# Kernel tuning notes

Hardware: AMD Instinct MI355X
Metric: run time of the kernel (lower is better)

## Reference

```python
import jax, jax.numpy as jnp
import numpy as np

D = 2048
NH = 16
DH = D // NH            # 128
DHR = DH // 2           # 64
DC = D // 2             # 1024
DCQ = D // 2            # 1024
B, L = 4, 2048
ROPE_BASE = 10000.0


def setup_inputs() -> dict:
    key = jax.random.key(0)
    ks = jax.random.split(key, 10)
    s = 0.02
    inp = {
        "x": jax.random.normal(ks[0], (B, L, D), dtype=jnp.float32),
        "W_DKV": jax.random.normal(ks[1], (D, DC), dtype=jnp.float32) * s,
        "W_UK": jax.random.normal(ks[2], (DC, NH * DH), dtype=jnp.float32) * s,
        "W_UV": jax.random.normal(ks[3], (DC, NH * DH), dtype=jnp.float32) * s,
        "W_DQ": jax.random.normal(ks[4], (D, DCQ), dtype=jnp.float32) * s,
        "W_UQ": jax.random.normal(ks[5], (DCQ, NH * DH), dtype=jnp.float32) * s,
        "W_QR": jax.random.normal(ks[6], (DCQ, NH * DHR), dtype=jnp.float32) * s,
        "W_KR": jax.random.normal(ks[7], (D, DHR), dtype=jnp.float32) * s,
        "W_O": jax.random.normal(ks[8], (D, D), dtype=jnp.float32) * s,
        "s_qk": jnp.asarray(np.sqrt(DH + DHR), dtype=jnp.float32),
    }
    return inp


def _rope_tables(seq_len, dim, dtype):
    # Standard rotate-half RoPE tables: cos/sin of shape (seq_len, dim)
    inv_freq = 1.0 / (ROPE_BASE ** (jnp.arange(0, dim, 2, dtype=jnp.float32) / dim))
    t = jnp.arange(seq_len, dtype=jnp.float32)
    freqs = jnp.outer(t, inv_freq)            # (L, dim/2)
    emb = jnp.concatenate([freqs, freqs], axis=-1)  # (L, dim)
    return jnp.cos(emb).astype(dtype), jnp.sin(emb).astype(dtype)


def _apply_rope(x, cos, sin):
    # x: (B, H, L, dim); cos/sin: (L, dim)
    half = x.shape[-1] // 2
    rot = jnp.concatenate([-x[..., half:], x[..., :half]], axis=-1)
    return x * cos[None, None] + rot * sin[None, None]


def reference(x, W_DKV, W_UK, W_UV, W_DQ, W_UQ, W_QR, W_KR, W_O, s_qk):
    Bb, Ll, Dd = x.shape
    cos, sin = _rope_tables(Ll, DHR, x.dtype)

    c_kv = x @ W_DKV                                            # (B,L,DC)
    k_c = (c_kv @ W_UK).reshape(Bb, Ll, NH, DH).transpose(0, 2, 1, 3)
    v = (c_kv @ W_UV).reshape(Bb, Ll, NH, DH).transpose(0, 2, 1, 3)

    c_q = x @ W_DQ                                              # (B,L,DCQ)
    q_c = (c_q @ W_UQ).reshape(Bb, Ll, NH, DH).transpose(0, 2, 1, 3)
    q_rope = _apply_rope((c_q @ W_QR).reshape(Bb, Ll, NH, DHR).transpose(0, 2, 1, 3), cos, sin)
    k_rope = _apply_rope((x @ W_KR).reshape(Bb, Ll, 1, DHR).transpose(0, 2, 1, 3), cos, sin)
    k_rope = jnp.broadcast_to(k_rope, (Bb, NH, Ll, DHR))

    q = jnp.concatenate([q_c, q_rope], axis=-1)                 # (B,H,L,DH+DHR)
    k = jnp.concatenate([k_c, k_rope], axis=-1)

    eps = 1e-12
    q = q / jnp.maximum(jnp.linalg.norm(q, axis=-1, keepdims=True), eps)
    k = k / jnp.maximum(jnp.linalg.norm(k, axis=-1, keepdims=True), eps)

    # SDPA with scale=1.0, causal mask, q pre-scaled by s_qk
    scores = jnp.einsum("bhqd,bhkd->bhqk", q * s_qk, k)         # (B,H,L,L)
    causal = jnp.tril(jnp.ones((Ll, Ll), dtype=bool))
    scores = jnp.where(causal[None, None], scores, jnp.finfo(scores.dtype).min)
    attn = jax.nn.softmax(scores, axis=-1)
    out = jnp.einsum("bhqk,bhkd->bhqd", attn, v)                # (B,H,L,DH)
    out = out.transpose(0, 2, 1, 3).reshape(Bb, Ll, Dd)
    return out @ W_O
```

## Files before the change

### kernel.cpp

```cpp
#include <hip/hip_runtime.h>
#include <stdint.h>

typedef unsigned short u16;
typedef unsigned int u32;
typedef short bf16x8 __attribute__((ext_vector_type(8)));
typedef float f32x4 __attribute__((ext_vector_type(4)));
typedef u16 u16x4 __attribute__((ext_vector_type(4)));

#define DEV __device__ __forceinline__

DEV float bf2f(u16 u) { union { float f; u32 i; } x; x.i = ((u32)u) << 16; return x.f; }
DEV u16 f2bf(float f) {
  union { float f; u32 i; } x; x.f = f;
  u32 i = x.i;
  u32 r = (i + 0x7fffu + ((i >> 16) & 1u)) >> 16;
  return (u16)r;
}

DEV void gl_lds16(const u16* g, u16* l) {
  __builtin_amdgcn_global_load_lds((const __attribute__((address_space(1))) u32*)g,
                                   (__attribute__((address_space(3))) u32*)l, 16, 0, 0);
}

__global__ __launch_bounds__(256) void cast_f32_bf16(const float* __restrict__ in,
                                                     u16* __restrict__ out, int n4) {
  int i = blockIdx.x * 256 + threadIdx.x;
  if (i >= n4) return;
  float4 v = ((const float4*)in)[i];
  u16x4 o;
  o.x = f2bf(v.x); o.y = f2bf(v.y); o.z = f2bf(v.z); o.w = f2bf(v.w);
  ((u16x4*)out)[i] = o;
}

__global__ __launch_bounds__(256) void transpose_cast(const float* __restrict__ W,
                                                      u16* __restrict__ Wt, int K, int N) {
  __shared__ float tile[64][65];
  int n0 = blockIdx.x * 64;
  int k0 = blockIdx.y * 64;
#pragma unroll
  for (int i = 0; i < 16; ++i) {
    int idx = threadIdx.x + i * 256;
    int r = idx >> 6, c = idx & 63;
    tile[r][c] = W[(size_t)(k0 + r) * N + n0 + c];
  }
  __syncthreads();
#pragma unroll
  for (int i = 0; i < 16; ++i) {
    int idx = threadIdx.x + i * 256;
    int r = idx >> 6, c = idx & 63;
    Wt[(size_t)(n0 + r) * K + k0 + c] = f2bf(tile[c][r]);
  }
}

__global__ __launch_bounds__(256) void transpose_v(const u16* __restrict__ KCV,
                                                   u16* __restrict__ Vt) {
  __shared__ float tile[64][65];
  int l0 = blockIdx.x * 64;
  int d0 = blockIdx.y * 64;
  int bh = blockIdx.z;
  int b = bh >> 4, h = bh & 15;
#pragma unroll
  for (int i = 0; i < 16; ++i) {
    int idx = threadIdx.x + i * 256;
    int r = idx >> 6, c = idx & 63;
    tile[r][c] = bf2f(KCV[(size_t)(b * 2048 + l0 + r) * 4096 + 2048 + h * 128 + d0 + c]);
  }
  __syncthreads();
#pragma unroll
  for (int i = 0; i < 16; ++i) {
    int idx = threadIdx.x + i * 256;
    int rr = idx >> 6, cc = idx & 63;
    Vt[((size_t)bh * 128 + d0 + rr) * 2048 + l0 + cc] = f2bf(tile[cc][rr]);
  }
}

DEV void ep_set(u16* E, int i, float v) { E[i] = f2bf(v); }
DEV void ep_set(float* E, int i, float v) { E[i] = v; }

template <typename OT>
__global__ __launch_bounds__(512, 2) void gemm256(const u16* __restrict__ A, int lda,
                                                  const u16* __restrict__ Bt,
                                                  OT* __restrict__ C, int ldc, int K) {
  __shared__ u16 smem[65536];
  const int tid = threadIdx.x;
  const int lane = tid & 63;
  const int w = tid >> 6;
  const int wm = w >> 2;
  const int wn = w & 3;
  const int quad = lane >> 4;
  const int l15 = lane & 15;
  const int cs = quad ^ ((l15 >> 1) & 3);
  const int nwg = gridDim.x * gridDim.y;
  const int lin = blockIdx.y * gridDim.x + blockIdx.x;
  const int swz = (lin & 7) * (nwg >> 3) + (lin >> 3);
  const int m0 = (swz / gridDim.x) * 256;
  const int n0 = (swz % gridDim.x) * 256;

  const int rloc = tid >> 2;
  const int clog = (tid & 3) ^ ((tid >> 3) & 3);
  const size_t aoff0 = (size_t)rloc * lda + clog * 8;
  const size_t boff0 = (size_t)rloc * (size_t)K + clog * 8;
  const u16* Ag = A + (size_t)m0 * lda;
  const u16* Bg = Bt + (size_t)n0 * K;

  auto stageA = [&](int u, int ks2) {
    u16* dst = smem + (u & 1) * 32768 + ks2 * 8192 + w * 512;
    const u16* s0 = Ag + aoff0 + u * 64 + ks2 * 32;
    gl_lds16(s0, dst);
    gl_lds16(s0 + (size_t)128 * lda, dst + 4096);
  };
  auto stageB = [&](int u, int ks2) {
    u16* dst = smem + (u & 1) * 32768 + 16384 + ks2 * 8192 + w * 512;
    const u16* s0 = Bg + boff0 + u * 64 + ks2 * 32;
    gl_lds16(s0, dst);
    gl_lds16(s0 + (size_t)128 * (size_t)K, dst + 4096);
  };

  f32x4 acc[2][4][4] = {};
  const int nt = K >> 6;

  stageA(0, 0); stageB(0, 0); stageA(0, 1); stageB(0, 1);
  stageA(1, 0); stageB(1, 0);
  asm volatile("s_waitcnt vmcnt(4)" ::: "memory");
  __builtin_amdgcn_s_barrier();

  for (int t = 0; t < nt; ++t) {
    const u16* As_ = smem + (t & 1) * 32768;
    const u16* Bs_ = As_ + 16384;
#pragma unroll
    for (int p = 0; p < 4; ++p) {
      const int ks = p >> 1;
      const int mq = p & 1;
      const u16* Ab = As_ + ks * 8192;
      const u16* Bb = Bs_ + ks * 8192;
      bf16x8 af[4], bf[4];
#pragma unroll
      for (int mt = 0; mt < 4; ++mt)
        af[mt] = *(const bf16x8*)&Ab[(wm * 128 + mq * 64 + mt * 16 + l15) * 32 + cs * 8];
#pragma unroll
      for (int n = 0; n < 4; ++n)
        bf[n] = *(const bf16x8*)&Bb[(wn * 64 + n * 16 + l15) * 32 + cs * 8];
      if (p == 0)      { if (t + 1 < nt) stageA(t + 1, 1); }
      else if (p == 1) { if (t + 1 < nt) stageB(t + 1, 1); }
      else if (p == 2) { if (t + 2 < nt) stageA(t + 2, 0); }
      else             { if (t + 2 < nt) stageB(t + 2, 0); }
      __builtin_amdgcn_s_barrier();
      __builtin_amdgcn_s_setprio(1);
#pragma unroll
      for (int mt = 0; mt < 4; ++mt)
#pragma unroll
        for (int n = 0; n < 4; ++n)
          acc[mq][mt][n] = __builtin_amdgcn_mfma_f32_16x16x32_bf16(af[mt], bf[n], acc[mq][mt][n], 0, 0, 0);
      __builtin_amdgcn_s_setprio(0);
      if (p == 3) asm volatile("s_waitcnt vmcnt(4)" ::: "memory");
      __builtin_amdgcn_s_barrier();
    }
  }
  asm volatile("s_waitcnt vmcnt(0)" ::: "memory");
  __builtin_amdgcn_s_barrier();

  OT* Ew = ((OT*)smem) + w * 1024;
#pragma unroll
  for (int mq = 0; mq < 2; ++mq) {
#pragma unroll
    for (int mt = 0; mt < 4; ++mt) {
#pragma unroll
      for (int n = 0; n < 4; ++n)
#pragma unroll
        for (int r = 0; r < 4; ++r)
          ep_set(Ew, (quad * 4 + r) * 64 + n * 16 + l15, acc[mq][mt][n][r]);
      asm volatile("s_waitcnt lgkmcnt(0)" ::: "memory");
#pragma unroll
      for (int it2 = 0; it2 < 4; ++it2) {
        int row_i = it2 * 4 + quad;
        size_t off = (size_t)(m0 + wm * 128 + mq * 64 + mt * 16 + row_i) * ldc + n0 + wn * 64 + l15 * 4;
        if constexpr (sizeof(OT) == 2) {
          *(u16x4*)&C[off] = *(const u16x4*)&Ew[row_i * 64 + l15 * 4];
        } else {
          *(float4*)&C[off] = *(const float4*)&Ew[row_i * 64 + l15 * 4];
        }
      }
      asm volatile("s_waitcnt lgkmcnt(0)" ::: "memory");
    }
  }
}

template <typename OT>
__global__ __launch_bounds__(256) void gemm_bt(const u16* __restrict__ A, int lda,
                                               const u16* __restrict__ Bt,
                                               OT* __restrict__ C, int ldc,
                                               int M, int N, int K) {
  __shared__ u16 smem_ab[2 * 128 * 32];
  u16* As = smem_ab;
  u16* Bs = smem_ab + 128 * 32;
  const int tid = threadIdx.x;
  const int lane = tid & 63;
  const int w = tid >> 6;
  const int quad = lane >> 4;
  const int l15 = lane & 15;
  const int nwg = gridDim.x * gridDim.y;
  const int lin = blockIdx.y * gridDim.x + blockIdx.x;
  const int swz = (lin & 7) * (nwg >> 3) + (lin >> 3);
  const int m0 = (swz / gridDim.x) * 128;
  const int n0 = (swz % gridDim.x) * 128;
  const int wm = (w & 1) * 64;
  const int wn = (w >> 1) * 64;

  f32x4 acc[4][4] = {};

  for (int k0 = 0; k0 < K; k0 += 32) {
#pragma unroll
    for (int it = 0; it < 2; ++it) {
      int ca = w * 128 + it * 64;
      int c = ca + lane;
      int row = c >> 2, kc = (c & 3) * 8;
      gl_lds16(A + (size_t)(m0 + row) * lda + k0 + kc, &As[ca * 8]);
      gl_lds16(Bt + (size_t)(n0 + row) * K + k0 + kc, &Bs[ca * 8]);
    }
    __syncthreads();
    bf16x8 af[4], bf[4];
#pragma unroll
    for (int mt = 0; mt < 4; ++mt) af[mt] = *(const bf16x8*)&As[(wm + mt * 16 + l15) * 32 + quad * 8];
#pragma unroll
    for (int nt = 0; nt < 4; ++nt) bf[nt] = *(const bf16x8*)&Bs[(wn + nt * 16 + l15) * 32 + quad * 8];
#pragma unroll
    for (int mt = 0; mt < 4; ++mt)
#pragma unroll
      for (int nt = 0; nt < 4; ++nt)
        acc[mt][nt] = __builtin_amdgcn_mfma_f32_16x16x32_bf16(af[mt], bf[nt], acc[mt][nt], 0, 0, 0);
    __syncthreads();
  }

  OT* Ew = ((OT*)smem_ab) + w * 1024;
#pragma unroll
  for (int mt = 0; mt < 4; ++mt) {
#pragma unroll
    for (int nt = 0; nt < 4; ++nt)
#pragma unroll
      for (int r = 0; r < 4; ++r)
        ep_set(Ew, (quad * 4 + r) * 64 + nt * 16 + l15, acc[mt][nt][r]);
    asm volatile("s_waitcnt lgkmcnt(0)" ::: "memory");
#pragma unroll
    for (int it2 = 0; it2 < 4; ++it2) {
      int row_i = it2 * 4 + quad;
      int colg = n0 + wn + l15 * 4;
      if (colg < N) {
        size_t off = (size_t)(m0 + wm + mt * 16 + row_i) * ldc + colg;
        if constexpr (sizeof(OT) == 2) {
          *(u16x4*)&C[off] = *(const u16x4*)&Ew[row_i * 64 + l15 * 4];
        } else {
          *(float4*)&C[off] = *(const float4*)&Ew[row_i * 64 + l15 * 4];
        }
      }
    }
    asm volatile("s_waitcnt lgkmcnt(0)" ::: "memory");
  }
}

__global__ __launch_bounds__(256) void build_q(const u16* __restrict__ qcr,
                                               const float* __restrict__ s_qk,
                                               u16* __restrict__ qn) {
  const int wid = blockIdx.x * 4 + (threadIdx.x >> 6);
  const int lane = threadIdx.x & 63;
  const int token = wid >> 4;
  const int h = wid & 15;
  const int b = token >> 11;
  const int l = token & 2047;
  float v0 = bf2f(qcr[(size_t)token * 3072 + h * 128 + lane]);
  float v1 = bf2f(qcr[(size_t)token * 3072 + h * 128 + 64 + lane]);
  int j = lane & 31;
  float freq = __expf((float)j * -0.28782313662425574f);
  float ang = (float)l * freq;
  float cs = __cosf(ang), sn = __sinf(ang);
  float xr = bf2f(qcr[(size_t)token * 3072 + 2048 + h * 64 + lane]);
  float xo = bf2f(qcr[(size_t)token * 3072 + 2048 + h * 64 + (lane ^ 32)]);
  float v2 = (lane < 32) ? (xr * cs - xo * sn) : (xr * cs + xo * sn);
  float ss = v0 * v0 + v1 * v1 + v2 * v2;
#pragma unroll
  for (int off = 1; off < 64; off <<= 1) ss += __shfl_xor(ss, off, 64);
  float scale = s_qk[0] / fmaxf(sqrtf(ss), 1e-12f);
  u16* out = qn + (((size_t)(b * 16 + h) * 2048) + l) * 192;
  out[lane] = f2bf(v0 * scale);
  out[64 + lane] = f2bf(v1 * scale);
  out[128 + lane] = f2bf(v2 * scale);
}

__global__ __launch_bounds__(256) void build_k(const u16* __restrict__ kcv,
                                               const u16* __restrict__ krr,
                                               u16* __restrict__ kn) {
  const int wid = blockIdx.x * 4 + (threadIdx.x >> 6);
  const int lane = threadIdx.x & 63;
  const int token = wid >> 4;
  const int h = wid & 15;
  const int b = token >> 11;
  const int l = token & 2047;
  float v0 = bf2f(kcv[(size_t)token * 4096 + h * 128 + lane]);
  float v1 = bf2f(kcv[(size_t)token * 4096 + h * 128 + 64 + lane]);
  int j = lane & 31;
  float freq = __expf((float)j * -0.28782313662425574f);
  float ang = (float)l * freq;
  float cs = __cosf(ang), sn = __sinf(ang);
  float xr = bf2f(krr[(size_t)token * 64 + lane]);
  float xo = bf2f(krr[(size_t)token * 64 + (lane ^ 32)]);
  float v2 = (lane < 32) ? (xr * cs - xo * sn) : (xr * cs + xo * sn);
  float ss = v0 * v0 + v1 * v1 + v2 * v2;
#pragma unroll
  for (int off = 1; off < 64; off <<= 1) ss += __shfl_xor(ss, off, 64);
  float scale = 1.0f / fmaxf(sqrtf(ss), 1e-12f);
  u16* out = kn + (((size_t)(b * 16 + h) * 2048) + l) * 192;
  out[lane] = f2bf(v0 * scale);
  out[64 + lane] = f2bf(v1 * scale);
  out[128 + lane] = f2bf(v2 * scale);
}

__global__ __launch_bounds__(512, 2) void flash_attn(const u16* __restrict__ Q,
                                                     const u16* __restrict__ Kn,
                                                     const u16* __restrict__ Vt,
                                                     const float* __restrict__ s_qk,
                                                     u16* __restrict__ O) {
  constexpr int L = 2048, DQK = 192, DV = 128, KVB = 64;
  constexpr int PSTR = 72;
  __shared__ u16 smem[59392];
  u16* KsBuf = smem;
  u16* VsBuf = smem + 24576;
  u16* Ps    = smem + 40960;
  const int tid = threadIdx.x;
  const int lane = tid & 63;
  const int w = tid >> 6;
  const int quad = lane >> 4;
  const int l15 = lane & 15;
  const int lin = blockIdx.x;
  const int xcd = lin & 7;
  const int g = lin >> 3;
  const int bh = ((g >> 2) << 3) | xcd;
  const int pairIdx = g & 3;
  const int b = bh >> 4, h = bh & 15;
  const float SMAX = s_qk[0];

  const u16* Kg = Kn + (size_t)bh * L * DQK;
  const u16* Vg = Vt + (size_t)bh * DV * L;

  auto stage = [&](int kt2, int bufi) {
    u16* KsB = KsBuf + bufi * 12288;
    u16* VsB = VsBuf + bufi * 8192;
#pragma unroll
    for (int it = 0; it < 5; ++it) {
      int B0 = it * 512 + w * 64;
      if (B0 < 1536) {
        int p = B0 + lane;
        int r = p / 24, cp = p % 24;
        int c = cp ^ (r & 7);
        gl_lds16(Kg + (size_t)(kt2 * KVB + r) * DQK + c * 8, &KsB[B0 * 8]);
      } else {
        int p = B0 - 1536 + lane;
        int dv = p >> 3, cp = p & 7;
        int c = cp ^ (dv & 7);
        gl_lds16(Vg + (size_t)dv * L + kt2 * KVB + c * 8, &VsB[(B0 - 1536) * 8]);
      }
    }
  };

  bf16x8 ones;
#pragma unroll
  for (int j = 0; j < 8; ++j) ones[j] = (short)0x3F80;

  for (int qp = 0; qp < 2; ++qp) {
    const int qt = (qp == 0) ? (7 - pairIdx) : pairIdx;
    const u16* Qg = Q + ((size_t)bh * L + qt * 256) * DQK;

    bf16x8 qf[2][6];
#pragma unroll
    for (int mt = 0; mt < 2; ++mt)
#pragma unroll
      for (int kd = 0; kd < 6; ++kd)
        qf[mt][kd] = *(const bf16x8*)&Qg[(w * 32 + mt * 16 + l15) * DQK + kd * 32 + quad * 8];

    f32x4 oacc[2][8] = {};
    f32x4 accL[2] = {};

    const int nkv = 4 * (qt + 1);
    stage(0, 0);
    __syncthreads();

    for (int kt = 0; kt < nkv; ++kt) {
      const int cur = kt & 1;
      if (kt + 1 < nkv) stage(kt + 1, cur ^ 1);
      const u16* KsC = KsBuf + cur * 12288;
      const u16* VsC = VsBuf + cur * 8192;

      f32x4 s[2][4] = {};
      __builtin_amdgcn_s_setprio(1);
#pragma unroll
      for (int kd = 0; kd < 6; ++kd) {
#pragma unroll
        for (int nt = 0; nt < 4; ++nt) {
          int row = nt * 16 + l15;
          int cp = (kd * 4 + quad) ^ (l15 & 7);
          bf16x8 bb = *(const bf16x8*)&KsC[row * DQK + cp * 8];
#pragma unroll
          for (int mt = 0; mt < 2; ++mt)
            s[mt][nt] = __builtin_amdgcn_mfma_f32_16x16x32_bf16(qf[mt][kd], bb, s[mt][nt], 0, 0, 0);
        }
      }
      __builtin_amdgcn_s_setprio(0);

      const int kcol0 = kt * KVB + l15;
      u16* Pw = &Ps[w * 32 * PSTR];
#pragma unroll
      for (int mt = 0; mt < 2; ++mt) {
        const int qrow_base = qt * 256 + w * 32 + mt * 16 + quad * 4;
#pragma unroll
        for (int r = 0; r < 4; ++r)
#pragma unroll
          for (int nt = 0; nt < 4; ++nt) {
            float p = (kcol0 + nt * 16 > qrow_base + r) ? 0.f : __expf(s[mt][nt][r] - SMAX);
            Pw[(mt * 16 + quad * 4 + r) * PSTR + nt * 16 + l15] = f2bf(p);
          }
      }
      asm volatile("s_waitcnt lgkmcnt(0)" ::: "memory");

      __builtin_amdgcn_s_setprio(1);
      bf16x8 pf[2][2];
#pragma unroll
      for (int mt = 0; mt < 2; ++mt)
#pragma unroll
        for (int kc = 0; kc < 2; ++kc) {
          pf[mt][kc] = *(const bf16x8*)&Pw[(mt * 16 + l15) * PSTR + kc * 32 + quad * 8];
          accL[mt] = __builtin_amdgcn_mfma_f32_16x16x32_bf16(pf[mt][kc], ones, accL[mt], 0, 0, 0);
        }
#pragma unroll
      for (int nt2 = 0; nt2 < 8; ++nt2) {
        const int dv = nt2 * 16 + l15;
#pragma unroll
        for (int kc = 0; kc < 2; ++kc) {
          int lc = (kc * 4 + quad) ^ (l15 & 7);
          bf16x8 vv = *(const bf16x8*)&VsC[dv * KVB + lc * 8];
#pragma unroll
          for (int mt = 0; mt < 2; ++mt)
            oacc[mt][nt2] = __builtin_amdgcn_mfma_f32_16x16x32_bf16(pf[mt][kc], vv, oacc[mt][nt2], 0, 0, 0);
        }
      }
      __builtin_amdgcn_s_setprio(0);
      __syncthreads();
    }

    float rinv[2][4];
#pragma unroll
    for (int mt = 0; mt < 2; ++mt)
#pragma unroll
      for (int r = 0; r < 4; ++r) rinv[mt][r] = 1.0f / accL[mt][r];
    u16* Ew = smem + w * 2048;
#pragma unroll
    for (int mt = 0; mt < 2; ++mt) {
#pragma unroll
      for (int nt2 = 0; nt2 < 8; ++nt2)
#pragma unroll
        for (int r = 0; r < 4; ++r)
          Ew[(quad * 4 + r) * 128 + nt2 * 16 + l15] = f2bf(oacc[mt][nt2][r] * rinv[mt][r]);
      asm volatile("s_waitcnt lgkmcnt(0)" ::: "memory");
#pragma unroll
      for (int it2 = 0; it2 < 4; ++it2) {
        int row_i = it2 * 4 + quad;
        int lg = qt * 256 + w * 32 + mt * 16 + row_i;
        uint4 v = *(const uint4*)&Ew[row_i * 128 + l15 * 8];
        *(uint4*)&O[((size_t)b * L + lg) * 2048 + h * 128 + l15 * 8] = v;
      }
      asm volatile("s_waitcnt lgkmcnt(0)" ::: "memory");
    }
    __syncthreads();
  }
}

extern "C" void kernel_launch(void* const* d_in, const int* in_sizes, int n_in,
                              void* d_out, int out_size, void* d_ws, size_t ws_size,
                              hipStream_t stream) {
  const float* x     = (const float*)d_in[0];
  const float* W_DKV = (const float*)d_in[1];
  const float* W_UK  = (const float*)d_in[2];
  const float* W_UV  = (const float*)d_in[3];
  const float* W_DQ  = (const float*)d_in[4];
  const float* W_UQ  = (const float*)d_in[5];
  const float* W_QR  = (const float*)d_in[6];
  const float* W_KR  = (const float*)d_in[7];
  const float* W_O   = (const float*)d_in[8];
  const float* s_qk  = (const float*)d_in[9];

  char* base = (char*)d_ws;
  u16* xb     = (u16*)(base);
  u16* WtDKVQ = (u16*)(base + (size_t)33554432);
  u16* WtUKV  = (u16*)(base + (size_t)41943040);
  u16* WtUQR  = (u16*)(base + (size_t)58720256);
  u16* WtKR   = (u16*)(base + (size_t)71303168);
  u16* WtO    = (u16*)(base + (size_t)71827456);
  u16* ckvq   = (u16*)(base + (size_t)80216064);
  u16* kcv    = (u16*)(base + (size_t)113770496);
  u16* qcr    = (u16*)(base + (size_t)180879360);
  u16* kr     = (u16*)(base + (size_t)231211008);
  u16* qn = (u16*)(base);
  u16* kn = qcr;
  u16* Vt = ckvq;
  u16* O  = kcv;

  cast_f32_bf16<<<16384, 256, 0, stream>>>(x, xb, 8192 * 2048 / 4);
  transpose_cast<<<dim3(16, 32), 256, 0, stream>>>(W_DKV, WtDKVQ,                  2048, 1024);
  transpose_cast<<<dim3(16, 32), 256, 0, stream>>>(W_DQ,  WtDKVQ + 1024 * 2048,    2048, 1024);
  transpose_cast<<<dim3(32, 16), 256, 0, stream>>>(W_UK,  WtUKV,                   1024, 2048);
  transpose_cast<<<dim3(32, 16), 256, 0, stream>>>(W_UV,  WtUKV + 2048 * 1024,     1024, 2048);
  transpose_cast<<<dim3(32, 16), 256, 0, stream>>>(W_UQ,  WtUQR,                   1024, 2048);
  transpose_cast<<<dim3(16, 16), 256, 0, stream>>>(W_QR,  WtUQR + 2048 * 1024,     1024, 1024);
  transpose_cast<<<dim3(1, 32),  256, 0, stream>>>(W_KR,  WtKR,                    2048, 64);
  transpose_cast<<<dim3(32, 32), 256, 0, stream>>>(W_O,   WtO,                     2048, 2048);

  gemm256<u16><<<dim3(8, 32),  512, 0, stream>>>(xb, 2048, WtDKVQ, ckvq, 2048, 2048);
  gemm_bt<u16><<<dim3(1, 64),  256, 0, stream>>>(xb, 2048, WtKR, kr, 64, 8192, 64, 2048);
  gemm256<u16><<<dim3(16, 32), 512, 0, stream>>>(ckvq, 2048, WtUKV, kcv, 4096, 1024);
  gemm256<u16><<<dim3(12, 32), 512, 0, stream>>>(ckvq + 1024, 2048, WtUQR, qcr, 3072, 1024);

  build_q<<<32768, 256, 0, stream>>>(qcr, s_qk, qn);
  build_k<<<32768, 256, 0, stream>>>(kcv, kr, kn);

  transpose_v<<<dim3(32, 2, 64), 256, 0, stream>>>(kcv, Vt);

  flash_attn<<<dim3(256), 512, 0, stream>>>(qn, kn, Vt, s_qk, O);

  gemm256<float><<<dim3(8, 32), 512, 0, stream>>>(O, 2048, WtO, (float*)d_out, 2048, 2048);
}
```

Baseline: 678.2 us.

## Fuse prep casts, merge projection GEMMs, and fold V transpose and Q norm

All input casts and weight transposes now run in a single prep kernel. The small W_KR projection is folded into the first GEMM as an extra zero-padded N tile, and the K/V/Q up-projections are merged into one GEMM launch. That GEMM writes V directly in transposed layout from its epilogue, so the separate transpose_v kernel goes away. The Q RoPE and normalization move into flash_attn's Q load, removing build_q and its intermediate buffer. The aim is fewer launches and less intermediate memory traffic, at the cost of extra per-tile Q work inside attention and more complex epilogues.

```diff
diff --git a/kernel.cpp b/kernel.cpp
--- a/kernel.cpp
+++ b/kernel.cpp
@@ -22,65 +22,77 @@
                                    (__attribute__((address_space(3))) u32*)l, 16, 0, 0);
 }
 
-__global__ __launch_bounds__(256) void cast_f32_bf16(const float* __restrict__ in,
-                                                     u16* __restrict__ out, int n4) {
-  int i = blockIdx.x * 256 + threadIdx.x;
-  if (i >= n4) return;
-  float4 v = ((const float4*)in)[i];
-  u16x4 o;
-  o.x = f2bf(v.x); o.y = f2bf(v.y); o.z = f2bf(v.z); o.w = f2bf(v.w);
-  ((u16x4*)out)[i] = o;
-}
-
-__global__ __launch_bounds__(256) void transpose_cast(const float* __restrict__ W,
-                                                      u16* __restrict__ Wt, int K, int N) {
+__global__ __launch_bounds__(256) void prep(const float* __restrict__ x,
+                                            const float* __restrict__ W_DKV,
+                                            const float* __restrict__ W_UK,
+                                            const float* __restrict__ W_UV,
+                                            const float* __restrict__ W_DQ,
+                                            const float* __restrict__ W_UQ,
+                                            const float* __restrict__ W_QR,
+                                            const float* __restrict__ W_KR,
+                                            const float* __restrict__ W_O,
+                                            u16* __restrict__ xb,
+                                            u16* __restrict__ WtDKVQ,
+                                            u16* __restrict__ WtUKV,
+                                            u16* __restrict__ WtO) {
   __shared__ float tile[64][65];
-  int n0 = blockIdx.x * 64;
-  int k0 = blockIdx.y * 64;
+  const int tid = threadIdx.x;
+  int bid = blockIdx.x;
+
+  if (bid < 4096) {
+#pragma unroll
+    for (int it = 0; it < 4; ++it) {
+      int i = bid * 1024 + it * 256 + tid;
+      float4 v = ((const float4*)x)[i];
+      u16x4 o;
+      o.x = f2bf(v.x); o.y = f2bf(v.y); o.z = f2bf(v.z); o.w = f2bf(v.w);
+      ((u16x4*)xb)[i] = o;
+    }
+    return;
+  }
+  bid -= 4096;
+
+  const float* W; u16* Wt; int K, N;
+  if (bid < 512)        { W = W_DKV; Wt = WtDKVQ;                K = 2048; N = 1024; }
+  else if (bid < 1024)  { W = W_DQ;  Wt = WtDKVQ + 1024 * 2048;  K = 2048; N = 1024; bid -= 512; }
+  else if (bid < 1536)  { W = W_UK;  Wt = WtUKV;                 K = 1024; N = 2048; bid -= 1024; }
+  else if (bid < 2048)  { W = W_UV;  Wt = WtUKV + 2048 * 1024;   K = 1024; N = 2048; bid -= 1536; }
+  else if (bid < 2560)  { W = W_UQ;  Wt = WtUKV + 4096 * 1024;   K = 1024; N = 2048; bid -= 2048; }
+  else if (bid < 2816)  { W = W_QR;  Wt = WtUKV + 6144 * 1024;   K = 1024; N = 1024; bid -= 2560; }
+  else if (bid < 2848)  { W = W_KR;  Wt = WtDKVQ + 2048 * 2048;  K = 2048; N = 64;   bid -= 2816; }
+  else if (bid < 3040) {
+    int i = (bid - 2848) * 256 + tid;
+    *(uint4*)&WtDKVQ[2112 * 2048 + i * 8] = uint4{0, 0, 0, 0};
+    return;
+  }
+  else                  { W = W_O;   Wt = WtO;                   K = 2048; N = 2048; bid -= 3040; }
+
+  const int gx = N >> 6;
+  const int n0 = (bid % gx) * 64;
+  const int k0 = (bid / gx) * 64;
 #pragma unroll
   for (int i = 0; i < 16; ++i) {
-    int idx = threadIdx.x + i * 256;
+    int idx = tid + i * 256;
     int r = idx >> 6, c = idx & 63;
     tile[r][c] = W[(size_t)(k0 + r) * N + n0 + c];
   }
   __syncthreads();
 #pragma unroll
   for (int i = 0; i < 16; ++i) {
-    int idx = threadIdx.x + i * 256;
+    int idx = tid + i * 256;
     int r = idx >> 6, c = idx & 63;
     Wt[(size_t)(n0 + r) * K + k0 + c] = f2bf(tile[c][r]);
   }
 }
 
-__global__ __launch_bounds__(256) void transpose_v(const u16* __restrict__ KCV,
-                                                   u16* __restrict__ Vt) {
-  __shared__ float tile[64][65];
-  int l0 = blockIdx.x * 64;
-  int d0 = blockIdx.y * 64;
-  int bh = blockIdx.z;
-  int b = bh >> 4, h = bh & 15;
-#pragma unroll
-  for (int i = 0; i < 16; ++i) {
-    int idx = threadIdx.x + i * 256;
-    int r = idx >> 6, c = idx & 63;
-    tile[r][c] = bf2f(KCV[(size_t)(b * 2048 + l0 + r) * 4096 + 2048 + h * 128 + d0 + c]);
-  }
-  __syncthreads();
-#pragma unroll
-  for (int i = 0; i < 16; ++i) {
-    int idx = threadIdx.x + i * 256;
-    int rr = idx >> 6, cc = idx & 63;
-    Vt[((size_t)bh * 128 + d0 + rr) * 2048 + l0 + cc] = f2bf(tile[cc][rr]);
-  }
-}
-
 DEV void ep_set(u16* E, int i, float v) { E[i] = f2bf(v); }
 DEV void ep_set(float* E, int i, float v) { E[i] = v; }
 
-template <typename OT>
+template <typename OT, int KIND>
 __global__ __launch_bounds__(512, 2) void gemm256(const u16* __restrict__ A, int lda,
                                                   const u16* __restrict__ Bt,
-                                                  OT* __restrict__ C, int ldc, int K) {
+                                                  OT* __restrict__ C, int ldc, int K,
+                                                  u16* __restrict__ X1, u16* __restrict__ X2) {
   __shared__ u16 smem[65536];
   const int tid = threadIdx.x;
   const int lane = tid & 63;
@@ -98,9 +110,10 @@
 
   const int rloc = tid >> 2;
   const int clog = (tid & 3) ^ ((tid >> 3) & 3);
+  const u16* Abase = A + ((KIND == 2 && n0 >= 4096) ? 1024 : 0);
   const size_t aoff0 = (size_t)rloc * lda + clog * 8;
   const size_t boff0 = (size_t)rloc * (size_t)K + clog * 8;
-  const u16* Ag = A + (size_t)m0 * lda;
+  const u16* Ag = Abase + (size_t)m0 * lda;
   const u16* Bg = Bt + (size_t)n0 * K;
 
   auto stageA = [&](int u, int ks2) {
@@ -159,6 +172,44 @@
   asm volatile("s_waitcnt vmcnt(0)" ::: "memory");
   __builtin_amdgcn_s_barrier();
 
+  if constexpr (KIND == 2) {
+    if (n0 >= 2048 && n0 < 4096) {
+      u16* Ewt = smem + w * 2560;
+      const int dvb = (n0 - 2048) + wn * 64;
+      const int hh = dvb >> 7;
+      const int dv0 = dvb & 127;
+#pragma unroll
+      for (int mq = 0; mq < 2; ++mq)
+#pragma unroll
+        for (int mh = 0; mh < 2; ++mh) {
+#pragma unroll
+          for (int mi = 0; mi < 2; ++mi)
+#pragma unroll
+            for (int n = 0; n < 4; ++n)
+#pragma unroll
+              for (int r = 0; r < 4; ++r)
+                Ewt[(n * 16 + l15) * 40 + mi * 16 + quad * 4 + r] = f2bf(acc[mq][mh * 2 + mi][n][r]);
+          asm volatile("s_waitcnt lgkmcnt(0)" ::: "memory");
+          const int mbase = m0 + wm * 128 + mq * 64 + mh * 32;
+          const int b_ = mbase >> 11, l_ = mbase & 2047;
+          u16* dstp = X1 + ((size_t)((b_ * 16 + hh) * 128 + dv0 + lane)) * 2048 + l_;
+          const u16* srcp = &Ewt[lane * 40];
+#pragma unroll
+          for (int k2 = 0; k2 < 4; ++k2)
+            *(uint4*)&dstp[k2 * 8] = *(const uint4*)&srcp[k2 * 8];
+          asm volatile("s_waitcnt lgkmcnt(0)" ::: "memory");
+        }
+      return;
+    }
+  }
+
+  OT* Cc = C; int ldcc = ldc, col0 = n0, Nlim = 1 << 30;
+  if constexpr (KIND == 1) {
+    if (n0 == 2048) { Cc = (OT*)X1; ldcc = 64; col0 = 0; Nlim = 64; }
+  }
+  if constexpr (KIND == 2) {
+    if (n0 >= 4096) { Cc = (OT*)X2; ldcc = 3072; col0 = n0 - 4096; }
+  }
   OT* Ew = ((OT*)smem) + w * 1024;
 #pragma unroll
   for (int mq = 0; mq < 2; ++mq) {
@@ -173,11 +224,14 @@
 #pragma unroll
       for (int it2 = 0; it2 < 4; ++it2) {
         int row_i = it2 * 4 + quad;
-        size_t off = (size_t)(m0 + wm * 128 + mq * 64 + mt * 16 + row_i) * ldc + n0 + wn * 64 + l15 * 4;
-        if constexpr (sizeof(OT) == 2) {
-          *(u16x4*)&C[off] = *(const u16x4*)&Ew[row_i * 64 + l15 * 4];
-        } else {
-          *(float4*)&C[off] = *(const float4*)&Ew[row_i * 64 + l15 * 4];
+        int colg = wn * 64 + l15 * 4;
+        if (colg < Nlim) {
+          size_t off = (size_t)(m0 + wm * 128 + mq * 64 + mt * 16 + row_i) * ldcc + col0 + colg;
+          if constexpr (sizeof(OT) == 2) {
+            *(u16x4*)&Cc[off] = *(const u16x4*)&Ew[row_i * 64 + l15 * 4];
+          } else {
+            *(float4*)&Cc[off] = *(const float4*)&Ew[row_i * 64 + l15 * 4];
+          }
         }
       }
       asm volatile("s_waitcnt lgkmcnt(0)" ::: "memory");
@@ -185,107 +239,7 @@
   }
 }
 
-template <typename OT>
-__global__ __launch_bounds__(256) void gemm_bt(const u16* __restrict__ A, int lda,
-                                               const u16* __restrict__ Bt,
-                                               OT* __restrict__ C, int ldc,
-                                               int M, int N, int K) {
-  __shared__ u16 smem_ab[2 * 128 * 32];
-  u16* As = smem_ab;
-  u16* Bs = smem_ab + 128 * 32;
-  const int tid = threadIdx.x;
-  const int lane = tid & 63;
-  const int w = tid >> 6;
-  const int quad = lane >> 4;
-  const int l15 = lane & 15;
-  const int nwg = gridDim.x * gridDim.y;
-  const int lin = blockIdx.y * gridDim.x + blockIdx.x;
-  const int swz = (lin & 7) * (nwg >> 3) + (lin >> 3);
-  const int m0 = (swz / gridDim.x) * 128;
-  const int n0 = (swz % gridDim.x) * 128;
-  const int wm = (w & 1) * 64;
-  const int wn = (w >> 1) * 64;
-
-  f32x4 acc[4][4] = {};
-
-  for (int k0 = 0; k0 < K; k0 += 32) {
-#pragma unroll
-    for (int it = 0; it < 2; ++it) {
-      int ca = w * 128 + it * 64;
-      int c = ca + lane;
-      int row = c >> 2, kc = (c & 3) * 8;
-      gl_lds16(A + (size_t)(m0 + row) * lda + k0 + kc, &As[ca * 8]);
-      gl_lds16(Bt + (size_t)(n0 + row) * K + k0 + kc, &Bs[ca * 8]);
-    }
-    __syncthreads();
-    bf16x8 af[4], bf[4];
-#pragma unroll
-    for (int mt = 0; mt < 4; ++mt) af[mt] = *(const bf16x8*)&As[(wm + mt * 16 + l15) * 32 + quad * 8];
-#pragma unroll
-    for (int nt = 0; nt < 4; ++nt) bf[nt] = *(const bf16x8*)&Bs[(wn + nt * 16 + l15) * 32 + quad * 8];
-#pragma unroll
-    for (int mt = 0; mt < 4; ++mt)
-#pragma unroll
-      for (int nt = 0; nt < 4; ++nt)
-        acc[mt][nt] = __builtin_amdgcn_mfma_f32_16x16x32_bf16(af[mt], bf[nt], acc[mt][nt], 0, 0, 0);
-    __syncthreads();
-  }
-
-  OT* Ew = ((OT*)smem_ab) + w * 1024;
-#pragma unroll
-  for (int mt = 0; mt < 4; ++mt) {
-#pragma unroll
-    for (int nt = 0; nt < 4; ++nt)
-#pragma unroll
-      for (int r = 0; r < 4; ++r)
-        ep_set(Ew, (quad * 4 + r) * 64 + nt * 16 + l15, acc[mt][nt][r]);
-    asm volatile("s_waitcnt lgkmcnt(0)" ::: "memory");
-#pragma unroll
-    for (int it2 = 0; it2 < 4; ++it2) {
-      int row_i = it2 * 4 + quad;
-      int colg = n0 + wn + l15 * 4;
-      if (colg < N) {
-        size_t off = (size_t)(m0 + wm + mt * 16 + row_i) * ldc + colg;
-        if constexpr (sizeof(OT) == 2) {
-          *(u16x4*)&C[off] = *(const u16x4*)&Ew[row_i * 64 + l15 * 4];
-        } else {
-          *(float4*)&C[off] = *(const float4*)&Ew[row_i * 64 + l15 * 4];
-        }
-      }
-    }
-    asm volatile("s_waitcnt lgkmcnt(0)" ::: "memory");
-  }
-}
-
-__global__ __launch_bounds__(256) void build_q(const u16* __restrict__ qcr,
-                                               const float* __restrict__ s_qk,
-                                               u16* __restrict__ qn) {
-  const int wid = blockIdx.x * 4 + (threadIdx.x >> 6);
-  const int lane = threadIdx.x & 63;
-  const int token = wid >> 4;
-  const int h = wid & 15;
-  const int b = token >> 11;
-  const int l = token & 2047;
-  float v0 = bf2f(qcr[(size_t)token * 3072 + h * 128 + lane]);
-  float v1 = bf2f(qcr[(size_t)token * 3072 + h * 128 + 64 + lane]);
-  int j = lane & 31;
-  float freq = __expf((float)j * -0.28782313662425574f);
-  float ang = (float)l * freq;
-  float cs = __cosf(ang), sn = __sinf(ang);
-  float xr = bf2f(qcr[(size_t)token * 3072 + 2048 + h * 64 + lane]);
-  float xo = bf2f(qcr[(size_t)token * 3072 + 2048 + h * 64 + (lane ^ 32)]);
-  float v2 = (lane < 32) ? (xr * cs - xo * sn) : (xr * cs + xo * sn);
-  float ss = v0 * v0 + v1 * v1 + v2 * v2;
-#pragma unroll
-  for (int off = 1; off < 64; off <<= 1) ss += __shfl_xor(ss, off, 64);
-  float scale = s_qk[0] / fmaxf(sqrtf(ss), 1e-12f);
-  u16* out = qn + (((size_t)(b * 16 + h) * 2048) + l) * 192;
-  out[lane] = f2bf(v0 * scale);
-  out[64 + lane] = f2bf(v1 * scale);
-  out[128 + lane] = f2bf(v2 * scale);
-}
-
-__global__ __launch_bounds__(256) void build_k(const u16* __restrict__ kcv,
+__global__ __launch_bounds__(256) void build_k(const u16* __restrict__ kc,
                                                const u16* __restrict__ krr,
                                                u16* __restrict__ kn) {
   const int wid = blockIdx.x * 4 + (threadIdx.x >> 6);
@@ -294,8 +248,8 @@
   const int h = wid & 15;
   const int b = token >> 11;
   const int l = token & 2047;
-  float v0 = bf2f(kcv[(size_t)token * 4096 + h * 128 + lane]);
-  float v1 = bf2f(kcv[(size_t)token * 4096 + h * 128 + 64 + lane]);
+  float v0 = bf2f(kc[(size_t)token * 2048 + h * 128 + lane]);
+  float v1 = bf2f(kc[(size_t)token * 2048 + h * 128 + 64 + lane]);
   int j = lane & 31;
   float freq = __expf((float)j * -0.28782313662425574f);
   float ang = (float)l * freq;
@@ -313,7 +267,7 @@
   out[128 + lane] = f2bf(v2 * scale);
 }
 
-__global__ __launch_bounds__(512, 2) void flash_attn(const u16* __restrict__ Q,
+__global__ __launch_bounds__(512, 2) void flash_attn(const u16* __restrict__ qcr,
                                                      const u16* __restrict__ Kn,
                                                      const u16* __restrict__ Vt,
                                                      const float* __restrict__ s_qk,
@@ -340,24 +294,31 @@
   const u16* Kg = Kn + (size_t)bh * L * DQK;
   const u16* Vg = Vt + (size_t)bh * DV * L;
 
+  int koffs[3], kdsts[3], voffs[2], vdsts[2];
+#pragma unroll
+  for (int it = 0; it < 3; ++it) {
+    int p = it * 512 + w * 64 + lane;
+    int r = p / 24, cp = p % 24;
+    koffs[it] = r * DQK + (cp ^ (r & 7)) * 8;
+    kdsts[it] = (it * 512 + w * 64) * 8;
+  }
+#pragma unroll
+  for (int it = 0; it < 2; ++it) {
+    int q = (it + 3) * 512 + w * 64 + lane - 1536;
+    int dv = q >> 3, cp = q & 7;
+    voffs[it] = dv * L + (cp ^ (dv & 7)) * 8;
+    vdsts[it] = ((it + 3) * 512 + w * 64 - 1536) * 8;
+  }
+
   auto stage = [&](int kt2, int bufi) {
     u16* KsB = KsBuf + bufi * 12288;
     u16* VsB = VsBuf + bufi * 8192;
-#pragma unroll
-    for (int it = 0; it < 5; ++it) {
-      int B0 = it * 512 + w * 64;
-      if (B0 < 1536) {
-        int p = B0 + lane;
-        int r = p / 24, cp = p % 24;
-        int c = cp ^ (r & 7);
-        gl_lds16(Kg + (size_t)(kt2 * KVB + r) * DQK + c * 8, &KsB[B0 * 8]);
-      } else {
-        int p = B0 - 1536 + lane;
-        int dv = p >> 3, cp = p & 7;
-        int c = cp ^ (dv & 7);
-        gl_lds16(Vg + (size_t)dv * L + kt2 * KVB + c * 8, &VsB[(B0 - 1536) * 8]);
-      }
-    }
+    const u16* Kt = Kg + (size_t)(kt2 * KVB) * DQK;
+    const u16* Vtb = Vg + kt2 * KVB;
+#pragma unroll
+    for (int it = 0; it < 3; ++it) gl_lds16(Kt + koffs[it], &KsB[kdsts[it]]);
+#pragma unroll
+    for (int it = 0; it < 2; ++it) gl_lds16(Vtb + voffs[it], &VsB[vdsts[it]]);
   };
 
   bf16x8 ones;
@@ -366,14 +327,49 @@
 
   for (int qp = 0; qp < 2; ++qp) {
     const int qt = (qp == 0) ? (7 - pairIdx) : pairIdx;
-    const u16* Qg = Q + ((size_t)bh * L + qt * 256) * DQK;
 
     bf16x8 qf[2][6];
 #pragma unroll
-    for (int mt = 0; mt < 2; ++mt)
-#pragma unroll
-      for (int kd = 0; kd < 6; ++kd)
-        qf[mt][kd] = *(const bf16x8*)&Qg[(w * 32 + mt * 16 + l15) * DQK + kd * 32 + quad * 8];
+    for (int mt = 0; mt < 2; ++mt) {
+      const int row = qt * 256 + w * 32 + mt * 16 + l15;
+      const u16* qr_ = qcr + (size_t)(b * 2048 + row) * 3072;
+#pragma unroll
+      for (int kd = 0; kd < 4; ++kd)
+        qf[mt][kd] = *(const bf16x8*)&qr_[h * 128 + kd * 32 + quad * 8];
+      bf16x8 a4 = *(const bf16x8*)&qr_[2048 + h * 64 + quad * 8];
+      bf16x8 a5 = *(const bf16x8*)&qr_[2048 + h * 64 + 32 + quad * 8];
+      float v4[8], v5[8];
+      float ss = 0.f;
+#pragma unroll
+      for (int e = 0; e < 8; ++e) {
+        int j = quad * 8 + e;
+        float fr = __expf((float)j * -0.28782313662425574f);
+        float ang = (float)row * fr;
+        float cs2 = __cosf(ang), sn2 = __sinf(ang);
+        float x4 = bf2f((u16)a4[e]), x5 = bf2f((u16)a5[e]);
+        v4[e] = x4 * cs2 - x5 * sn2;
+        v5[e] = x5 * cs2 + x4 * sn2;
+        ss += v4[e] * v4[e] + v5[e] * v5[e];
+      }
+#pragma unroll
+      for (int kd = 0; kd < 4; ++kd)
+#pragma unroll
+        for (int e = 0; e < 8; ++e) { float xv = bf2f((u16)qf[mt][kd][e]); ss += xv * xv; }
+      ss += __shfl_xor(ss, 16, 64);
+      ss += __shfl_xor(ss, 32, 64);
+      float scale = SMAX / fmaxf(sqrtf(ss), 1e-12f);
+#pragma unroll
+      for (int kd = 0; kd < 4; ++kd) {
+        bf16x8 t = qf[mt][kd];
+#pragma unroll
+        for (int e = 0; e < 8; ++e) t[e] = (short)f2bf(bf2f((u16)t[e]) * scale);
+        qf[mt][kd] = t;
+      }
+      bf16x8 t4, t5;
+#pragma unroll
+      for (int e = 0; e < 8; ++e) { t4[e] = (short)f2bf(v4[e] * scale); t5[e] = (short)f2bf(v5[e] * scale); }
+      qf[mt][4] = t4; qf[mt][5] = t5;
+    }
 
     f32x4 oacc[2][8] = {};
     f32x4 accL[2] = {};
@@ -424,20 +420,20 @@
 #pragma unroll
       for (int mt = 0; mt < 2; ++mt)
 #pragma unroll
-        for (int kc = 0; kc < 2; ++kc) {
-          pf[mt][kc] = *(const bf16x8*)&Pw[(mt * 16 + l15) * PSTR + kc * 32 + quad * 8];
-          accL[mt] = __builtin_amdgcn_mfma_f32_16x16x32_bf16(pf[mt][kc], ones, accL[mt], 0, 0, 0);
+        for (int kc2 = 0; kc2 < 2; ++kc2) {
+          pf[mt][kc2] = *(const bf16x8*)&Pw[(mt * 16 + l15) * PSTR + kc2 * 32 + quad * 8];
+          accL[mt] = __builtin_amdgcn_mfma_f32_16x16x32_bf16(pf[mt][kc2], ones, accL[mt], 0, 0, 0);
         }
 #pragma unroll
       for (int nt2 = 0; nt2 < 8; ++nt2) {
         const int dv = nt2 * 16 + l15;
 #pragma unroll
-        for (int kc = 0; kc < 2; ++kc) {
-          int lc = (kc * 4 + quad) ^ (l15 & 7);
+        for (int kc2 = 0; kc2 < 2; ++kc2) {
+          int lc = (kc2 * 4 + quad) ^ (l15 & 7);
           bf16x8 vv = *(const bf16x8*)&VsC[dv * KVB + lc * 8];
 #pragma unroll
           for (int mt = 0; mt < 2; ++mt)
-            oacc[mt][nt2] = __builtin_amdgcn_mfma_f32_16x16x32_bf16(pf[mt][kc], vv, oacc[mt][nt2], 0, 0, 0);
+            oacc[mt][nt2] = __builtin_amdgcn_mfma_f32_16x16x32_bf16(pf[mt][kc2], vv, oacc[mt][nt2], 0, 0, 0);
         }
       }
       __builtin_amdgcn_s_setprio(0);
@@ -488,40 +484,27 @@
   char* base = (char*)d_ws;
   u16* xb     = (u16*)(base);
   u16* WtDKVQ = (u16*)(base + (size_t)33554432);
-  u16* WtUKV  = (u16*)(base + (size_t)41943040);
-  u16* WtUQR  = (u16*)(base + (size_t)58720256);
-  u16* WtKR   = (u16*)(base + (size_t)71303168);
-  u16* WtO    = (u16*)(base + (size_t)71827456);
-  u16* ckvq   = (u16*)(base + (size_t)80216064);
-  u16* kcv    = (u16*)(base + (size_t)113770496);
-  u16* qcr    = (u16*)(base + (size_t)180879360);
-  u16* kr     = (u16*)(base + (size_t)231211008);
-  u16* qn = (u16*)(base);
-  u16* kn = qcr;
-  u16* Vt = ckvq;
-  u16* O  = kcv;
-
-  cast_f32_bf16<<<16384, 256, 0, stream>>>(x, xb, 8192 * 2048 / 4);
-  transpose_cast<<<dim3(16, 32), 256, 0, stream>>>(W_DKV, WtDKVQ,                  2048, 1024);
-  transpose_cast<<<dim3(16, 32), 256, 0, stream>>>(W_DQ,  WtDKVQ + 1024 * 2048,    2048, 1024);
-  transpose_cast<<<dim3(32, 16), 256, 0, stream>>>(W_UK,  WtUKV,                   1024, 2048);
-  transpose_cast<<<dim3(32, 16), 256, 0, stream>>>(W_UV,  WtUKV + 2048 * 1024,     1024, 2048);
-  transpose_cast<<<dim3(32, 16), 256, 0, stream>>>(W_UQ,  WtUQR,                   1024, 2048);
-  transpose_cast<<<dim3(16, 16), 256, 0, stream>>>(W_QR,  WtUQR + 2048 * 1024,     1024, 1024);
-  transpose_cast<<<dim3(1, 32),  256, 0, stream>>>(W_KR,  WtKR,                    2048, 64);
-  transpose_cast<<<dim3(32, 32), 256, 0, stream>>>(W_O,   WtO,                     2048, 2048);
-
-  gemm256<u16><<<dim3(8, 32),  512, 0, stream>>>(xb, 2048, WtDKVQ, ckvq, 2048, 2048);
-  gemm_bt<u16><<<dim3(1, 64),  256, 0, stream>>>(xb, 2048, WtKR, kr, 64, 8192, 64, 2048);
-  gemm256<u16><<<dim3(16, 32), 512, 0, stream>>>(ckvq, 2048, WtUKV, kcv, 4096, 1024);
-  gemm256<u16><<<dim3(12, 32), 512, 0, stream>>>(ckvq + 1024, 2048, WtUQR, qcr, 3072, 1024);
-
-  build_q<<<32768, 256, 0, stream>>>(qcr, s_qk, qn);
-  build_k<<<32768, 256, 0, stream>>>(kcv, kr, kn);
-
-  transpose_v<<<dim3(32, 2, 64), 256, 0, stream>>>(kcv, Vt);
-
-  flash_attn<<<dim3(256), 512, 0, stream>>>(qn, kn, Vt, s_qk, O);
-
-  gemm256<float><<<dim3(8, 32), 512, 0, stream>>>(O, 2048, WtO, (float*)d_out, 2048, 2048);
-}
+  u16* WtUKV  = (u16*)(base + (size_t)42991616);
+  u16* WtO    = (u16*)(base + (size_t)57671680);
+  u16* ckvq   = (u16*)(base + (size_t)66060288);
+  u16* kc     = (u16*)(base + (size_t)99614720);
+  u16* Vt     = (u16*)(base + (size_t)133169152);
+  u16* qcr    = (u16*)(base + (size_t)166723584);
+  u16* kr     = (u16*)(base + (size_t)217055232);
+  u16* kn = (u16*)(base);
+  u16* O  = ckvq;
+
+  prep<<<8160, 256, 0, stream>>>(x, W_DKV, W_UK, W_UV, W_DQ, W_UQ, W_QR, W_KR, W_O,
+                                 xb, WtDKVQ, WtUKV, WtO);
+
+  gemm256<u16, 1><<<dim3(9, 32), 512, 0, stream>>>(xb, 2048, WtDKVQ, ckvq, 2048, 2048, kr, nullptr);
+
+  gemm256<u16, 2><<<dim3(28, 32), 512, 0, stream>>>(ckvq, 2048, WtUKV, kc, 2048, 1024, Vt, qcr);
+
+  build_k<<<32768, 256, 0, stream>>>(kc, kr, kn);
+
+  flash_attn<<<dim3(256), 512, 0, stream>>>(qcr, kn, Vt, s_qk, O);
+
+  gemm256<float, 0><<<dim3(8, 32), 512, 0, stream>>>(O, 2048, WtO, (float*)d_out, 2048, 2048,
+                                                     nullptr, nullptr);
+}
```

Result: faster. 623.1 us (-8.1%).
